# Performance work log

Hardware: AMD Instinct MI355X
Metric: run time of the kernel (lower is better)

The kernel has to match this reference:

```python
import jax, jax.numpy as jnp
import numpy as np

VOCAB, EMB, HID = 32000, 256, 256
B, T = 2, 512


def setup_inputs() -> dict:
    key = jax.random.key(0)
    ks = jax.random.split(key, 16)
    s_e = 1.0 / np.sqrt(EMB)
    s_h = 1.0 / np.sqrt(HID)
    inp = {
        "x": jax.random.randint(ks[0], (B, T), 0, VOCAB),
        "emb": jax.random.normal(ks[1], (VOCAB, EMB), jnp.float32),
        # PyTorch LSTM params, gate order (i, f, g, o)
        "W_ih": jax.random.uniform(ks[2], (4 * HID, EMB), jnp.float32, -s_h, s_h),
        "W_hh": jax.random.uniform(ks[3], (4 * HID, HID), jnp.float32, -s_h, s_h),
        "b_ih": jax.random.uniform(ks[4], (4 * HID,), jnp.float32, -s_h, s_h),
        "b_hh": jax.random.uniform(ks[5], (4 * HID,), jnp.float32, -s_h, s_h),
        "W1": jax.random.uniform(ks[6], (HID, HID), jnp.float32, -s_h, s_h),
        "b1": jax.random.uniform(ks[7], (HID,), jnp.float32, -s_h, s_h),
        "W2": jax.random.uniform(ks[8], (HID, HID), jnp.float32, -s_h, s_h),
        "b2": jax.random.uniform(ks[9], (HID,), jnp.float32, -s_h, s_h),
        "V": jax.random.uniform(ks[10], (1, HID), jnp.float32, -s_h, s_h),
        "bV": jax.random.uniform(ks[11], (1,), jnp.float32, -s_h, s_h),
        "Wfc": jax.random.uniform(ks[12], (VOCAB, 2 * HID), jnp.float32, -s_h / np.sqrt(2), s_h / np.sqrt(2)),
        "bfc": jax.random.uniform(ks[13], (VOCAB,), jnp.float32, -s_h / np.sqrt(2), s_h / np.sqrt(2)),
    }
    return inp


def _lstm(xe, W_ih, W_hh, b_ih, b_hh):
    # xe: (B, T, E) -> outputs (B, T, H)
    Bv, Tv, _ = xe.shape
    H = W_hh.shape[1]
    # precompute input contributions for all timesteps
    gx = jnp.einsum('bte,ge->btg', xe, W_ih) + b_ih + b_hh  # (B, T, 4H)
    gx = jnp.transpose(gx, (1, 0, 2))  # (T, B, 4H)

    def step(carry, g_t):
        h, c = carry
        g = g_t + h @ W_hh.T
        i, f, gg, o = jnp.split(g, 4, axis=-1)
        i = jax.nn.sigmoid(i)
        f = jax.nn.sigmoid(f)
        gg = jnp.tanh(gg)
        o = jax.nn.sigmoid(o)
        c = f * c + i * gg
        h = o * jnp.tanh(c)
        return (h, c), h

    h0 = jnp.zeros((Bv, H), xe.dtype)
    c0 = jnp.zeros((Bv, H), xe.dtype)
    _, hs = jax.lax.scan(step, (h0, c0), gx)
    return jnp.transpose(hs, (1, 0, 2))  # (B, T, H)


def reference(x, emb, W_ih, W_hh, b_ih, b_hh, W1, b1, W2, b2, V, bV, Wfc, bfc):
    xe = emb[x]  # (B, T, E)
    outputs = _lstm(xe, W_ih, W_hh, b_ih, b_hh)  # (B, T, H)
    Tv = outputs.shape[1]
    a = outputs @ W1.T + b1  # (B, T, H) -> query side (i)
    b = outputs @ W2.T + b2  # (B, T, H) -> key side (j)
    # score[b, i, j] = V . tanh(a[b, i] + b[b, j]) + bV
    s = jnp.tanh(a[:, :, None, :] + b[:, None, :, :])  # (B, T, T, H)
    score = jnp.einsum('bijh,h->bij', s, V[0]) + bV[0]  # (B, T, T)
    causal = jnp.tril(jnp.ones((Tv, Tv), bool))
    score = jnp.where(causal[None], score, -jnp.inf)
    attn = jax.nn.softmax(score, axis=-1)  # (B, T, T)
    context = jnp.einsum('bij,bjh->bih', attn, outputs)  # (B, T, H)
    combined = jnp.concatenate([outputs, context], axis=-1)  # (B, T, 2H)
    logits = combined @ Wfc.T + bfc  # (B, T, VOCAB)
    return logits
```

## Files before the change

### kernel.cpp

```cpp
#include <hip/hip_runtime.h>
#include <stdint.h>

#define B_   2
#define T_   512
#define E_   256
#define H_   256
#define VOC  32000
#define G4   1024

#define SENT 0x7f800001u

#define OFF_GX    0u
#define OFF_H     4194304u
#define OFF_PROJ  5244928u
#define OFF_SCORE 7342080u
#define OFF_ABF   9439232u
#define OFF_WBF   10487808u

typedef __attribute__((ext_vector_type(8))) short short8;
typedef __attribute__((ext_vector_type(4))) float f32x4;

__device__ __forceinline__ unsigned short f2bf(float f) {
    unsigned u = __float_as_uint(f);
    unsigned r = (u + 0x7FFFu + ((u >> 16) & 1u)) >> 16;
    return (unsigned short)r;
}
__device__ __forceinline__ float sigmoid_f(float x) {
    return 1.0f / (1.0f + __expf(-x));
}
__device__ __forceinline__ float tanh_f(float x) {
    float e = __expf(-2.0f * fabsf(x));
    float t = (1.0f - e) / (1.0f + e);
    return (x >= 0.0f) ? t : -t;
}

__global__ __launch_bounds__(256) void k_init(unsigned* hbuf) {
    int idx = blockIdx.x * 256 + threadIdx.x;
    if (idx < 513 * 2 * 256) hbuf[idx] = (idx < 2 * 256) ? 0u : SENT;
}

__global__ __launch_bounds__(256) void k_embed_gx(const int* __restrict__ x,
                                                  const float* __restrict__ emb,
                                                  const float* __restrict__ Wih,
                                                  const float* __restrict__ bih,
                                                  const float* __restrict__ bhh,
                                                  float* __restrict__ gx) {
    __shared__ float As[64 * 65];
    __shared__ float Bs[64 * 65];
    int t = threadIdx.x;
    int n0 = blockIdx.x * 64, m0 = blockIdx.y * 64;
    int ty = t >> 4, tx = t & 15;
    float c[4][4] = {};
    for (int kc = 0; kc < E_; kc += 64) {
        __syncthreads();
        #pragma unroll
        for (int i = 0; i < 4; ++i) {
            int f = i * 256 + t;
            int r = f >> 4, c4 = f & 15;
            int xi = x[m0 + r];
            float4 av = *(const float4*)(emb + (size_t)xi * E_ + kc + c4 * 4);
            As[r * 65 + c4 * 4 + 0] = av.x; As[r * 65 + c4 * 4 + 1] = av.y;
            As[r * 65 + c4 * 4 + 2] = av.z; As[r * 65 + c4 * 4 + 3] = av.w;
            float4 bv = *(const float4*)(Wih + (size_t)(n0 + r) * E_ + kc + c4 * 4);
            Bs[r * 65 + c4 * 4 + 0] = bv.x; Bs[r * 65 + c4 * 4 + 1] = bv.y;
            Bs[r * 65 + c4 * 4 + 2] = bv.z; Bs[r * 65 + c4 * 4 + 3] = bv.w;
        }
        __syncthreads();
        for (int k = 0; k < 64; ++k) {
            float a[4], b[4];
            #pragma unroll
            for (int ii = 0; ii < 4; ++ii) a[ii] = As[(ty * 4 + ii) * 65 + k];
            #pragma unroll
            for (int jj = 0; jj < 4; ++jj) b[jj] = Bs[(tx * 4 + jj) * 65 + k];
            #pragma unroll
            for (int ii = 0; ii < 4; ++ii)
                #pragma unroll
                for (int jj = 0; jj < 4; ++jj)
                    c[ii][jj] = fmaf(a[ii], b[jj], c[ii][jj]);
        }
    }
    #pragma unroll
    for (int ii = 0; ii < 4; ++ii)
        #pragma unroll
        for (int jj = 0; jj < 4; ++jj) {
            int m = m0 + ty * 4 + ii, n = n0 + tx * 4 + jj;
            gx[(size_t)m * G4 + n] = c[ii][jj] + bih[n] + bhh[n];
        }
}

__global__ __launch_bounds__(512) void k_lstm(const float* __restrict__ Whh,
                                              const float* __restrict__ gx,
                                              float* hbuf,
                                              const float* __restrict__ Wfc,
                                              unsigned short* __restrict__ Wbf) {
    int bid = blockIdx.x;
    int role = bid & 7;
    int t = threadIdx.x;
    if (role >= 2) {
        int c = (bid >> 3) * 6 + role - 2;
        const float4* src = (const float4*)Wfc;
        ushort4* dst = (ushort4*)Wbf;
        for (int idx = c * 512 + t; idx < VOC * 512 / 4; idx += 24 * 512) {
            float4 v = src[idx];
            ushort4 o;
            o.x = f2bf(v.x); o.y = f2bf(v.y); o.z = f2bf(v.z); o.w = f2bf(v.w);
            dst[idx] = o;
        }
        return;
    }
    int beta = role;
    int q = bid >> 3;
    __shared__ float hs[256];
    __shared__ float p[256];
    int rl = t >> 1, half = t & 1;
    int g = rl >> 6, u = rl & 63;
    int row = g * 256 + q * 64 + u;
    float w[128];
    #pragma unroll
    for (int k = 0; k < 32; ++k) {
        float4 wv = *(const float4*)(Whh + (size_t)row * 256 + half * 128 + k * 4);
        w[k * 4 + 0] = wv.x; w[k * 4 + 1] = wv.y; w[k * 4 + 2] = wv.z; w[k * 4 + 3] = wv.w;
    }
    float c_reg = 0.0f;
    const float* gxb = gx + (size_t)beta * T_ * G4;
    unsigned* hb = (unsigned*)hbuf;
    for (int s = 0; s < T_; ++s) {
        float gxv = (half == 0) ? gxb[(size_t)s * G4 + row] : 0.0f;
        if (t < 256) {
            unsigned* pp = hb + (s * 2 + beta) * 256 + t;
            unsigned v;
            do {
                v = __hip_atomic_load(pp, __ATOMIC_RELAXED, __HIP_MEMORY_SCOPE_AGENT);
            } while (v == SENT);
            hs[t] = __uint_as_float(v);
        }
        __syncthreads();
        float acc = gxv;
        #pragma unroll
        for (int kk = 0; kk < 32; ++kk) {
            float4 h4 = *(const float4*)(hs + half * 128 + kk * 4);
            acc = fmaf(w[kk * 4 + 0], h4.x, acc);
            acc = fmaf(w[kk * 4 + 1], h4.y, acc);
            acc = fmaf(w[kk * 4 + 2], h4.z, acc);
            acc = fmaf(w[kk * 4 + 3], h4.w, acc);
        }
        acc += __shfl_xor(acc, 1);
        if (half == 0) p[rl] = acc;
        __syncthreads();
        if (t < 64) {
            float pi = p[t], pf = p[64 + t], pg = p[128 + t], po = p[192 + t];
            float ig = sigmoid_f(pi), fg = sigmoid_f(pf);
            float gg = tanh_f(pg),    og = sigmoid_f(po);
            c_reg = fmaf(fg, c_reg, ig * gg);
            float h = og * tanh_f(c_reg);
            __hip_atomic_store(hb + ((s + 1) * 2 + beta) * 256 + q * 64 + t,
                               __float_as_uint(h),
                               __ATOMIC_RELAXED, __HIP_MEMORY_SCOPE_AGENT);
        }
    }
}

__global__ __launch_bounds__(256) void k_proj(const float* __restrict__ hbuf,
                                              const float* __restrict__ W1,
                                              const float* __restrict__ b1,
                                              const float* __restrict__ W2,
                                              const float* __restrict__ b2,
                                              float* __restrict__ proj) {
    __shared__ float As[64 * 65];
    __shared__ float Bs[64 * 65];
    int t = threadIdx.x;
    int n0 = blockIdx.x * 64, m0 = blockIdx.y * 64;
    int ty = t >> 4, tx = t & 15;
    float c[4][4] = {};
    for (int kc = 0; kc < H_; kc += 64) {
        __syncthreads();
        #pragma unroll
        for (int i = 0; i < 4; ++i) {
            int f = i * 256 + t;
            int r = f >> 4, c4 = f & 15;
            int m = m0 + r; int bb = m >> 9, tl = m & 511;
            float4 av = *(const float4*)(hbuf + ((size_t)(tl + 1) * 2 + bb) * H_ + kc + c4 * 4);
            As[r * 65 + c4 * 4 + 0] = av.x; As[r * 65 + c4 * 4 + 1] = av.y;
            As[r * 65 + c4 * 4 + 2] = av.z; As[r * 65 + c4 * 4 + 3] = av.w;
            int n = n0 + r;
            const float* Wp = (n < 256) ? (W1 + (size_t)n * H_) : (W2 + (size_t)(n - 256) * H_);
            float4 bv = *(const float4*)(Wp + kc + c4 * 4);
            Bs[r * 65 + c4 * 4 + 0] = bv.x; Bs[r * 65 + c4 * 4 + 1] = bv.y;
            Bs[r * 65 + c4 * 4 + 2] = bv.z; Bs[r * 65 + c4 * 4 + 3] = bv.w;
        }
        __syncthreads();
        for (int k = 0; k < 64; ++k) {
            float a[4], b[4];
            #pragma unroll
            for (int ii = 0; ii < 4; ++ii) a[ii] = As[(ty * 4 + ii) * 65 + k];
            #pragma unroll
            for (int jj = 0; jj < 4; ++jj) b[jj] = Bs[(tx * 4 + jj) * 65 + k];
            #pragma unroll
            for (int ii = 0; ii < 4; ++ii)
                #pragma unroll
                for (int jj = 0; jj < 4; ++jj)
                    c[ii][jj] = fmaf(a[ii], b[jj], c[ii][jj]);
        }
    }
    #pragma unroll
    for (int ii = 0; ii < 4; ++ii)
        #pragma unroll
        for (int jj = 0; jj < 4; ++jj) {
            int m = m0 + ty * 4 + ii, n = n0 + tx * 4 + jj;
            float bias = (n < 256) ? b1[n] : b2[n - 256];
            proj[(size_t)m * 512 + n] = c[ii][jj] + bias;
        }
}

__global__ __launch_bounds__(256) void k_scores(const float* __restrict__ proj,
                                                const float* __restrict__ V,
                                                const float* __restrict__ bV,
                                                float* __restrict__ score) {
    int jt = blockIdx.x, it = blockIdx.y, b = blockIdx.z;
    if (jt > it) return;
    __shared__ float aT[16 * 260];
    __shared__ float bT[16 * 260];
    __shared__ float Vs[256];
    int t = threadIdx.x;
    int i0 = it * 16, j0 = jt * 16;
    #pragma unroll
    for (int i = 0; i < 4; ++i) {
        int f = i * 256 + t;
        int r = f >> 6, c4 = f & 63;
        *(float4*)(aT + r * 260 + c4 * 4) =
            *(const float4*)(proj + (size_t)(b * 512 + i0 + r) * 512 + c4 * 4);
        *(float4*)(bT + r * 260 + c4 * 4) =
            *(const float4*)(proj + (size_t)(b * 512 + j0 + r) * 512 + 256 + c4 * 4);
    }
    Vs[t] = V[t];
    __syncthreads();
    int ti = t >> 4, tj = t & 15;
    float sc = 0.0f;
    #pragma unroll 4
    for (int c4 = 0; c4 < 64; ++c4) {
        float4 av = *(const float4*)(aT + ti * 260 + c4 * 4);
        float4 bv = *(const float4*)(bT + tj * 260 + c4 * 4);
        float4 vv = *(const float4*)(Vs + c4 * 4);
        sc = fmaf(vv.x, tanh_f(av.x + bv.x), sc);
        sc = fmaf(vv.y, tanh_f(av.y + bv.y), sc);
        sc = fmaf(vv.z, tanh_f(av.z + bv.z), sc);
        sc = fmaf(vv.w, tanh_f(av.w + bv.w), sc);
    }
    score[(size_t)(b * 512 + i0 + ti) * 512 + j0 + tj] = sc + bV[0];
}

__global__ __launch_bounds__(256) void k_softctx(const float* __restrict__ hbuf,
                                                 const float* __restrict__ score,
                                                 unsigned short* __restrict__ Abf) {
    int i = blockIdx.x, b = blockIdx.y;
    int t = threadIdx.x;
    __shared__ float pe[512];
    __shared__ float r1[4];
    __shared__ float r2[4];
    const float* srow = score + (size_t)(b * 512 + i) * 512;
    float s1 = (t <= i) ? srow[t] : -1e30f;
    float s2 = (t + 256 <= i) ? srow[t + 256] : -1e30f;
    float mx = fmaxf(s1, s2);
    for (int off = 32; off; off >>= 1) mx = fmaxf(mx, __shfl_xor(mx, off));
    int wid = t >> 6, lane = t & 63;
    if (lane == 0) r1[wid] = mx;
    __syncthreads();
    mx = fmaxf(fmaxf(r1[0], r1[1]), fmaxf(r1[2], r1[3]));
    float e1 = (t <= i) ? __expf(s1 - mx) : 0.0f;
    float e2 = (t + 256 <= i) ? __expf(s2 - mx) : 0.0f;
    pe[t] = e1; pe[t + 256] = e2;
    float sm = e1 + e2;
    for (int off = 32; off; off >>= 1) sm += __shfl_xor(sm, off);
    if (lane == 0) r2[wid] = sm;
    __syncthreads();
    sm = r2[0] + r2[1] + r2[2] + r2[3];
    float inv = 1.0f / sm;
    float acc = 0.0f;
    int n = i + 1;
    #pragma unroll 4
    for (int j = 0; j < n; ++j)
        acc = fmaf(pe[j], hbuf[(size_t)(j + 1) * 512 + b * 256 + t], acc);
    float ctx = acc * inv;
    float outv = hbuf[(size_t)(i + 1) * 512 + b * 256 + t];
    size_t m = (size_t)b * 512 + i;
    Abf[m * 512 + t]       = f2bf(outv);
    Abf[m * 512 + 256 + t] = f2bf(ctx);
}

__global__ __launch_bounds__(256) void k_fc(const unsigned short* __restrict__ Abf,
                                            const unsigned short* __restrict__ Wbf,
                                            const float* __restrict__ bfc,
                                            float* __restrict__ out) {
    __shared__ uint4 AsV[1024];
    __shared__ uint4 BsV[1024];
    char* As = (char*)AsV;
    char* Bs = (char*)BsV;
    int t = threadIdx.x;
    int n0 = blockIdx.x * 128, m0 = blockIdx.y * 128;
    int wid = t >> 6, lane = t & 63;
    int wr = wid >> 1, wc = wid & 1;
    f32x4 acc[4][4];
    #pragma unroll
    for (int a = 0; a < 4; ++a)
        #pragma unroll
        for (int bq = 0; bq < 4; ++bq)
            #pragma unroll
            for (int r = 0; r < 4; ++r) acc[a][bq][r] = 0.0f;

    uint4 ra[4], rb[4];
    auto loadk = [&](int kt) {
        #pragma unroll
        for (int i = 0; i < 4; ++i) {
            int chunk = i * 256 + t, row = chunk >> 3, c8 = chunk & 7;
            ra[i] = *(const uint4*)(Abf + (size_t)(m0 + row) * 512 + kt * 64 + c8 * 8);
            rb[i] = *(const uint4*)(Wbf + (size_t)(n0 + row) * 512 + kt * 64 + c8 * 8);
        }
    };
    loadk(0);
    for (int kt = 0; kt < 8; ++kt) {
        __syncthreads();
        #pragma unroll
        for (int i = 0; i < 4; ++i) {
            int chunk = i * 256 + t, row = chunk >> 3, c8 = chunk & 7;
            int db = row * 128 + ((c8 ^ (row & 7)) << 4);
            *(uint4*)(As + db) = ra[i];
            *(uint4*)(Bs + db) = rb[i];
        }
        __syncthreads();
        if (kt < 7) loadk(kt + 1);
        #pragma unroll
        for (int kk = 0; kk < 2; ++kk) {
            short8 av[4], bv[4];
            #pragma unroll
            for (int mi = 0; mi < 4; ++mi) {
                int rowl = wr * 64 + mi * 16 + (lane & 15);
                int c8 = kk * 4 + (lane >> 4);
                av[mi] = *(const short8*)(As + rowl * 128 + ((c8 ^ (rowl & 7)) << 4));
            }
            #pragma unroll
            for (int ni = 0; ni < 4; ++ni) {
                int rowl = wc * 64 + ni * 16 + (lane & 15);
                int c8 = kk * 4 + (lane >> 4);
                bv[ni] = *(const short8*)(Bs + rowl * 128 + ((c8 ^ (rowl & 7)) << 4));
            }
            #pragma unroll
            for (int mi = 0; mi < 4; ++mi)
                #pragma unroll
                for (int ni = 0; ni < 4; ++ni)
                    acc[mi][ni] = __builtin_amdgcn_mfma_f32_16x16x32_bf16(
                        av[mi], bv[ni], acc[mi][ni], 0, 0, 0);
        }
    }
    #pragma unroll
    for (int ni = 0; ni < 4; ++ni) {
        int col = n0 + wc * 64 + ni * 16 + (lane & 15);
        float bias = bfc[col];
        #pragma unroll
        for (int mi = 0; mi < 4; ++mi) {
            int rowb = m0 + wr * 64 + mi * 16 + ((lane >> 4) << 2);
            #pragma unroll
            for (int r = 0; r < 4; ++r)
                out[(size_t)(rowb + r) * VOC + col] = acc[mi][ni][r] + bias;
        }
    }
}

extern "C" void kernel_launch(void* const* d_in, const int* in_sizes, int n_in,
                              void* d_out, int out_size, void* d_ws, size_t ws_size,
                              hipStream_t stream) {
    const int*   x   = (const int*)  d_in[0];
    const float* emb = (const float*)d_in[1];
    const float* Wih = (const float*)d_in[2];
    const float* Whh = (const float*)d_in[3];
    const float* bih = (const float*)d_in[4];
    const float* bhh = (const float*)d_in[5];
    const float* W1  = (const float*)d_in[6];
    const float* b1  = (const float*)d_in[7];
    const float* W2  = (const float*)d_in[8];
    const float* b2  = (const float*)d_in[9];
    const float* V   = (const float*)d_in[10];
    const float* bV  = (const float*)d_in[11];
    const float* Wfc = (const float*)d_in[12];
    const float* bfc = (const float*)d_in[13];
    float* out = (float*)d_out;

    char* ws = (char*)d_ws;
    float* gx            = (float*)(ws + OFF_GX);
    float* hbuf          = (float*)(ws + OFF_H);
    float* proj          = (float*)(ws + OFF_PROJ);
    float* score         = (float*)(ws + OFF_SCORE);
    unsigned short* Abf  = (unsigned short*)(ws + OFF_ABF);
    unsigned short* Wbf  = (unsigned short*)(ws + OFF_WBF);

    k_init    <<<dim3(1026),       dim3(256), 0, stream>>>((unsigned*)hbuf);
    k_embed_gx<<<dim3(16, 16),     dim3(256), 0, stream>>>(x, emb, Wih, bih, bhh, gx);
    k_lstm    <<<dim3(32),         dim3(512), 0, stream>>>(Whh, gx, hbuf, Wfc, Wbf);
    k_proj    <<<dim3(8, 16),      dim3(256), 0, stream>>>(hbuf, W1, b1, W2, b2, proj);
    k_scores  <<<dim3(32, 32, 2),  dim3(256), 0, stream>>>(proj, V, bV, score);
    k_softctx <<<dim3(512, 2),     dim3(256), 0, stream>>>(hbuf, score, Abf);
    k_fc      <<<dim3(250, 8),     dim3(256), 0, stream>>>(Abf, Wbf, bfc, out);
}
```

Measured before the change: 1.316 ms.

## Run each batch's LSTM recurrence in one block with fp16 register weights

```diff
diff --git a/kernel.cpp b/kernel.cpp
--- a/kernel.cpp
+++ b/kernel.cpp
@@ -8,8 +8,6 @@
 #define VOC  32000
 #define G4   1024
 
-#define SENT 0x7f800001u
-
 #define OFF_GX    0u
 #define OFF_H     4194304u
 #define OFF_PROJ  5244928u
@@ -19,6 +17,24 @@
 
 typedef __attribute__((ext_vector_type(8))) short short8;
 typedef __attribute__((ext_vector_type(4))) float f32x4;
+typedef _Float16 half2_t __attribute__((ext_vector_type(2)));
+
+#if defined(__has_builtin)
+#  if __has_builtin(__builtin_amdgcn_fdot2)
+#    define HAVE_FDOT2 1
+#  endif
+#endif
+
+__device__ __forceinline__ half2_t u2h(unsigned u) {
+    union { unsigned u; half2_t h; } x; x.u = u; return x.h;
+}
+__device__ __forceinline__ float dot2f(half2_t a, half2_t b, float c) {
+#ifdef HAVE_FDOT2
+    return __builtin_amdgcn_fdot2(a, b, c, false);
+#else
+    return fmaf((float)a.x, (float)b.x, fmaf((float)a.y, (float)b.y, c));
+#endif
+}
 
 __device__ __forceinline__ unsigned short f2bf(float f) {
     unsigned u = __float_as_uint(f);
@@ -32,11 +48,6 @@
     float e = __expf(-2.0f * fabsf(x));
     float t = (1.0f - e) / (1.0f + e);
     return (x >= 0.0f) ? t : -t;
-}
-
-__global__ __launch_bounds__(256) void k_init(unsigned* hbuf) {
-    int idx = blockIdx.x * 256 + threadIdx.x;
-    if (idx < 513 * 2 * 256) hbuf[idx] = (idx < 2 * 256) ? 0u : SENT;
 }
 
 __global__ __launch_bounds__(256) void k_embed_gx(const int* __restrict__ x,
@@ -90,17 +101,16 @@
 
 __global__ __launch_bounds__(512) void k_lstm(const float* __restrict__ Whh,
                                               const float* __restrict__ gx,
-                                              float* hbuf,
+                                              float* __restrict__ hbuf,
                                               const float* __restrict__ Wfc,
                                               unsigned short* __restrict__ Wbf) {
     int bid = blockIdx.x;
-    int role = bid & 7;
-    int t = threadIdx.x;
-    if (role >= 2) {
-        int c = (bid >> 3) * 6 + role - 2;
+    int t = threadIdx.x;
+    if (bid >= 2) {
+        int cidx = (bid - 2) * 512 + t;
         const float4* src = (const float4*)Wfc;
         ushort4* dst = (ushort4*)Wbf;
-        for (int idx = c * 512 + t; idx < VOC * 512 / 4; idx += 24 * 512) {
+        for (int idx = cidx; idx < VOC * 512 / 4; idx += 128 * 512) {
             float4 v = src[idx];
             ushort4 o;
             o.x = f2bf(v.x); o.y = f2bf(v.y); o.z = f2bf(v.z); o.w = f2bf(v.w);
@@ -108,54 +118,59 @@
         }
         return;
     }
-    int beta = role;
-    int q = bid >> 3;
-    __shared__ float hs[256];
-    __shared__ float p[256];
-    int rl = t >> 1, half = t & 1;
-    int g = rl >> 6, u = rl & 63;
-    int row = g * 256 + q * 64 + u;
-    float w[128];
-    #pragma unroll
-    for (int k = 0; k < 32; ++k) {
-        float4 wv = *(const float4*)(Whh + (size_t)row * 256 + half * 128 + k * 4);
-        w[k * 4 + 0] = wv.x; w[k * 4 + 1] = wv.y; w[k * 4 + 2] = wv.z; w[k * 4 + 3] = wv.w;
-    }
+    int beta = bid;
+    __shared__ half2_t h16s[128];
+    __shared__ float ps[1024];
+    int rowA = t, rowB = t + 512;
+
+    half2_t wA[128], wB[128];
+    #pragma unroll
+    for (int k4 = 0; k4 < 64; ++k4) {
+        float4 wv = *(const float4*)(Whh + (size_t)rowA * 256 + k4 * 4);
+        half2_t p0; p0.x = (_Float16)wv.x; p0.y = (_Float16)wv.y;
+        half2_t p1; p1.x = (_Float16)wv.z; p1.y = (_Float16)wv.w;
+        wA[k4 * 2] = p0; wA[k4 * 2 + 1] = p1;
+        float4 wu = *(const float4*)(Whh + (size_t)rowB * 256 + k4 * 4);
+        half2_t q0; q0.x = (_Float16)wu.x; q0.y = (_Float16)wu.y;
+        half2_t q1; q1.x = (_Float16)wu.z; q1.y = (_Float16)wu.w;
+        wB[k4 * 2] = q0; wB[k4 * 2 + 1] = q1;
+    }
+    if (t < 128) ((unsigned*)h16s)[t] = 0u;
     float c_reg = 0.0f;
     const float* gxb = gx + (size_t)beta * T_ * G4;
-    unsigned* hb = (unsigned*)hbuf;
+    float gA = gxb[rowA], gB = gxb[rowB];
+
     for (int s = 0; s < T_; ++s) {
-        float gxv = (half == 0) ? gxb[(size_t)s * G4 + row] : 0.0f;
+        __syncthreads();
+        float accA = gA, accB = gB;
+        if (s + 1 < T_) {
+            gA = gxb[(size_t)(s + 1) * G4 + rowA];
+            gB = gxb[(size_t)(s + 1) * G4 + rowB];
+        }
+        const uint4* hv4 = (const uint4*)h16s;
+        #pragma unroll
+        for (int kk = 0; kk < 32; ++kk) {
+            uint4 hc = hv4[kk];
+            accA = dot2f(u2h(hc.x), wA[kk * 4 + 0], accA);
+            accB = dot2f(u2h(hc.x), wB[kk * 4 + 0], accB);
+            accA = dot2f(u2h(hc.y), wA[kk * 4 + 1], accA);
+            accB = dot2f(u2h(hc.y), wB[kk * 4 + 1], accB);
+            accA = dot2f(u2h(hc.z), wA[kk * 4 + 2], accA);
+            accB = dot2f(u2h(hc.z), wB[kk * 4 + 2], accB);
+            accA = dot2f(u2h(hc.w), wA[kk * 4 + 3], accA);
+            accB = dot2f(u2h(hc.w), wB[kk * 4 + 3], accB);
+        }
+        ps[rowA] = accA;
+        ps[rowB] = accB;
+        __syncthreads();
         if (t < 256) {
-            unsigned* pp = hb + (s * 2 + beta) * 256 + t;
-            unsigned v;
-            do {
-                v = __hip_atomic_load(pp, __ATOMIC_RELAXED, __HIP_MEMORY_SCOPE_AGENT);
-            } while (v == SENT);
-            hs[t] = __uint_as_float(v);
-        }
-        __syncthreads();
-        float acc = gxv;
-        #pragma unroll
-        for (int kk = 0; kk < 32; ++kk) {
-            float4 h4 = *(const float4*)(hs + half * 128 + kk * 4);
-            acc = fmaf(w[kk * 4 + 0], h4.x, acc);
-            acc = fmaf(w[kk * 4 + 1], h4.y, acc);
-            acc = fmaf(w[kk * 4 + 2], h4.z, acc);
-            acc = fmaf(w[kk * 4 + 3], h4.w, acc);
-        }
-        acc += __shfl_xor(acc, 1);
-        if (half == 0) p[rl] = acc;
-        __syncthreads();
-        if (t < 64) {
-            float pi = p[t], pf = p[64 + t], pg = p[128 + t], po = p[192 + t];
+            float pi = ps[t], pf = ps[t + 256], pg = ps[t + 512], po = ps[t + 768];
             float ig = sigmoid_f(pi), fg = sigmoid_f(pf);
             float gg = tanh_f(pg),    og = sigmoid_f(po);
             c_reg = fmaf(fg, c_reg, ig * gg);
             float h = og * tanh_f(c_reg);
-            __hip_atomic_store(hb + ((s + 1) * 2 + beta) * 256 + q * 64 + t,
-                               __float_as_uint(h),
-                               __ATOMIC_RELAXED, __HIP_MEMORY_SCOPE_AGENT);
+            ((_Float16*)h16s)[t] = (_Float16)h;
+            hbuf[((size_t)(s + 1) * 2 + beta) * 256 + t] = h;
         }
     }
 }
@@ -392,9 +407,8 @@
     unsigned short* Abf  = (unsigned short*)(ws + OFF_ABF);
     unsigned short* Wbf  = (unsigned short*)(ws + OFF_WBF);
 
-    k_init    <<<dim3(1026),       dim3(256), 0, stream>>>((unsigned*)hbuf);
     k_embed_gx<<<dim3(16, 16),     dim3(256), 0, stream>>>(x, emb, Wih, bih, bhh, gx);
-    k_lstm    <<<dim3(32),         dim3(512), 0, stream>>>(Whh, gx, hbuf, Wfc, Wbf);
+    k_lstm    <<<dim3(130),        dim3(512), 0, stream>>>(Whh, gx, hbuf, Wfc, Wbf);
     k_proj    <<<dim3(8, 16),      dim3(256), 0, stream>>>(hbuf, W1, b1, W2, b2, proj);
     k_scores  <<<dim3(32, 32, 2),  dim3(256), 0, stream>>>(proj, V, bV, score);
     k_softctx <<<dim3(512, 2),     dim3(256), 0, stream>>>(hbuf, score, Abf);
```

Result: slower. 2.518 ms (+91.4%).
